# Kernel optimization log

Measured on AMD Instinct MI355X. Metric: run time of the kernel, lower is better.

The kernel has to match this reference:

```python
import jax, jax.numpy as jnp
import numpy as np

B, S, D, V, L = 8, 8192, 768, 64, 26  # batch, seq, hidden, symbol vocab, labels


def setup_inputs() -> dict:
    key = jax.random.key(0)
    k1, k2, k3 = jax.random.split(key, 3)
    hidden_states = jax.random.normal(k1, (B, S, D), dtype=jnp.float32)
    input_ids = jax.random.randint(k2, (B, S), 0, V, dtype=jnp.int32)
    W = jax.random.normal(k3, (L, D), dtype=jnp.float32) * 0.02
    b = jnp.zeros((L,), dtype=jnp.float32)
    return {"hidden_states": hidden_states, "W": W, "b": b, "input_ids": input_ids}


def reference(hidden_states, W, b, input_ids):
    # Per-batch, per-symbol mean pooling of hidden states, then linear classify.
    # Dense/padded equivalent of the torch per-symbol boolean-mask loop:
    # row (batch_b, symbol_v) = classifier(mean of hidden_states[b] where input_ids[b]==v),
    # masked to 0 for symbol 0 and for symbols absent in the sequence.
    Bv, Sv, Dv = hidden_states.shape
    seg = (input_ids + jnp.arange(Bv, dtype=input_ids.dtype)[:, None] * V).reshape(-1)
    flat_h = hidden_states.reshape(-1, Dv)
    sums = jax.ops.segment_sum(flat_h, seg, num_segments=Bv * V)            # [B*V, D]
    counts = jax.ops.segment_sum(
        jnp.ones((Bv * Sv,), dtype=hidden_states.dtype), seg, num_segments=Bv * V
    )                                                                        # [B*V]
    means = sums / jnp.maximum(counts, 1.0)[:, None]
    logits = means @ W.T + b                                                 # [B*V, L]
    present = (counts > 0) & ((jnp.arange(Bv * V) % V) > 0)                  # exclude symbol 0
    logits = jnp.where(present[:, None], logits, 0.0)
    return logits.reshape(Bv, V, -1)
```

## Files before the change

### kernel.cpp

```cpp
#include <hip/hip_runtime.h>

#define B_ 8
#define S_ 8192
#define D_ 768
#define V_ 64
#define L_ 26

typedef __attribute__((ext_vector_type(8))) short short8;
typedef __attribute__((ext_vector_type(4))) float floatx4;

#define TOKS 256
#define NSL  48

__global__ __launch_bounds__(256) void pool_mfma_kernel(
    const float* __restrict__ h, const int* __restrict__ ids,
    float* __restrict__ gsum)
{
    const int tid  = threadIdx.x;
    const int lane = tid & 63;
    const int wave = tid >> 6;
    const int nl   = lane & 15;
    const int quad = lane >> 4;

    const int b  = blockIdx.z;
    const int k0 = blockIdx.x * TOKS;
    const int n0 = blockIdx.y * (4 * NSL) + wave * NSL;

    const int*   idrow = ids + b * S_ + k0;
    const float* hrow  = h + ((size_t)b * S_ + k0) * D_ + n0;

    floatx4 acc[4][3];
    #pragma unroll
    for (int mt = 0; mt < 4; ++mt)
        #pragma unroll
        for (int nt = 0; nt < 3; ++nt) acc[mt][nt] = (floatx4)0.f;

    for (int ks = 0; ks < TOKS; ks += 32) {
        const int kb = ks + quad * 8;
        const int4* ip = (const int4*)(idrow + kb);
        const int4 i0 = ip[0], i1 = ip[1];
        const int idv[8] = {i0.x, i0.y, i0.z, i0.w, i1.x, i1.y, i1.z, i1.w};

        short8 afrag[4];
        #pragma unroll
        for (int mt = 0; mt < 4; ++mt) {
            const int m = mt * 16 + nl;
            #pragma unroll
            for (int j = 0; j < 8; ++j)
                afrag[mt][j] = (idv[j] == m) ? (short)0x3F80 : (short)0;
        }

        #pragma unroll
        for (int nt = 0; nt < 3; ++nt) {
            const float* bp = hrow + (size_t)kb * D_ + nt * 16 + nl;
            float f[8];
            #pragma unroll
            for (int j = 0; j < 8; ++j) f[j] = bp[(size_t)j * D_];
            short8 bhi, blo;
            #pragma unroll
            for (int j = 0; j < 8; ++j) {
                const unsigned u = __builtin_bit_cast(unsigned, f[j]);
                bhi[j] = (short)(u >> 16);
                const float hif = __builtin_bit_cast(float, u & 0xFFFF0000u);
                const float lof = f[j] - hif;
                blo[j] = (short)(__builtin_bit_cast(unsigned, lof) >> 16);
            }
            #pragma unroll
            for (int mt = 0; mt < 4; ++mt) {
                acc[mt][nt] = __builtin_amdgcn_mfma_f32_16x16x32_bf16(
                    afrag[mt], bhi, acc[mt][nt], 0, 0, 0);
                acc[mt][nt] = __builtin_amdgcn_mfma_f32_16x16x32_bf16(
                    afrag[mt], blo, acc[mt][nt], 0, 0, 0);
            }
        }
    }

    #pragma unroll
    for (int mt = 0; mt < 4; ++mt)
        #pragma unroll
        for (int nt = 0; nt < 3; ++nt)
            #pragma unroll
            for (int r = 0; r < 4; ++r) {
                const int v = mt * 16 + quad * 4 + r;
                const int d = n0 + nt * 16 + nl;
                unsafeAtomicAdd(&gsum[((size_t)b * V_ + v) * D_ + d],
                                acc[mt][nt][r]);
            }
}

__global__ __launch_bounds__(256) void hist_kernel(
    const int* __restrict__ ids, unsigned int* __restrict__ gcnt)
{
    __shared__ unsigned int cnt[V_];
    const int tid = threadIdx.x;
    const int b   = blockIdx.x >> 3;
    const int seg = blockIdx.x & 7;
    if (tid < V_) cnt[tid] = 0u;
    __syncthreads();
    const int per = S_ / 8;
    const int4* p = (const int4*)(ids + b * S_ + seg * per);
    for (int i = tid; i < per / 4; i += 256) {
        const int4 q = p[i];
        atomicAdd(&cnt[q.x], 1u); atomicAdd(&cnt[q.y], 1u);
        atomicAdd(&cnt[q.z], 1u); atomicAdd(&cnt[q.w], 1u);
    }
    __syncthreads();
    if (tid < V_ && cnt[tid]) atomicAdd(&gcnt[b * V_ + tid], cnt[tid]);
}

__global__ __launch_bounds__(256) void finalize_kernel(
    const float* __restrict__ gsum, const unsigned int* __restrict__ gcnt,
    const float* __restrict__ Wm, const float* __restrict__ bias,
    float* __restrict__ out)
{
    const int bv   = blockIdx.x;
    const int v    = bv & (V_ - 1);
    const int lane = threadIdx.x & 63;
    const int wave = threadIdx.x >> 6;

    const unsigned int c = gcnt[bv];
    const float inv = 1.f / (float)(c > 1u ? c : 1u);
    const bool present = (c > 0u) && (v > 0);

    float m[12];
    const float* srow = gsum + (size_t)bv * D_;
    #pragma unroll
    for (int j = 0; j < 12; ++j) m[j] = srow[lane + 64 * j] * inv;

    const int l0 = wave * 7;
    const int l1 = (l0 + 7 < L_) ? (l0 + 7) : L_;
    for (int l = l0; l < l1; ++l) {
        const float* wrow = Wm + l * D_;
        float p = 0.f;
        #pragma unroll
        for (int j = 0; j < 12; ++j) p += m[j] * wrow[lane + 64 * j];
        #pragma unroll
        for (int off = 32; off > 0; off >>= 1) p += __shfl_down(p, off);
        if (lane == 0) out[bv * L_ + l] = present ? (p + bias[l]) : 0.f;
    }
}

extern "C" void kernel_launch(void* const* d_in, const int* in_sizes, int n_in,
                              void* d_out, int out_size, void* d_ws, size_t ws_size,
                              hipStream_t stream) {
    const float* h    = (const float*)d_in[0];
    const float* Wm   = (const float*)d_in[1];
    const float* bias = (const float*)d_in[2];
    const int*   ids  = (const int*)d_in[3];
    float* out = (float*)d_out;

    float* gsum = (float*)d_ws;
    unsigned int* gcnt = (unsigned int*)(gsum + (size_t)B_ * V_ * D_);
    const size_t ws_needed = (size_t)B_ * V_ * D_ * sizeof(float)
                           + (size_t)B_ * V_ * sizeof(unsigned int);

    hipMemsetAsync(d_ws, 0, ws_needed, stream);

    hist_kernel<<<B_ * 8, 256, 0, stream>>>(ids, gcnt);

    dim3 grid1(S_ / TOKS, D_ / (4 * NSL), B_);
    pool_mfma_kernel<<<grid1, 256, 0, stream>>>(h, ids, gsum);

    finalize_kernel<<<B_ * V_, 256, 0, stream>>>(gsum, gcnt, Wm, bias, out);
}
```

Baseline: 313.5 us.

## Replace global atomics with per-slice partials and fuse histogram into pooling

The pooling kernel now writes per-slice partial sums into a workspace instead of doing global float atomics, which also removes the memset. It doubles tokens per block. The separate histogram kernel is folded into the pooling kernel, with per-slice counts written by the blockIdx.y==0 blocks. A new reduce-finalize kernel sums the 16 slices, computes means in shared memory and applies the classifier. The aim is to cut atomic contention and two launches, at the cost of extra partial-buffer traffic (16x B*V*D floats) and fewer blocks in the pooling grid.

```diff
diff --git a/kernel.cpp b/kernel.cpp
--- a/kernel.cpp
+++ b/kernel.cpp
@@ -9,25 +9,41 @@
 typedef __attribute__((ext_vector_type(8))) short short8;
 typedef __attribute__((ext_vector_type(4))) float floatx4;
 
-#define TOKS 256
+#define TOKS 512
+#define SLICES (S_ / TOKS)
 #define NSL  48
 
-__global__ __launch_bounds__(256) void pool_mfma_kernel(
+__global__ __launch_bounds__(256, 2) void pool_mfma_kernel(
     const float* __restrict__ h, const int* __restrict__ ids,
-    float* __restrict__ gsum)
+    float* __restrict__ part, unsigned int* __restrict__ cntpart)
 {
+    __shared__ unsigned int cnt[V_];
+
     const int tid  = threadIdx.x;
     const int lane = tid & 63;
     const int wave = tid >> 6;
     const int nl   = lane & 15;
     const int quad = lane >> 4;
 
-    const int b  = blockIdx.z;
-    const int k0 = blockIdx.x * TOKS;
-    const int n0 = blockIdx.y * (4 * NSL) + wave * NSL;
+    const int b     = blockIdx.z;
+    const int slice = blockIdx.x;
+    const int k0    = slice * TOKS;
+    const int n0    = blockIdx.y * (4 * NSL) + wave * NSL;
 
     const int*   idrow = ids + b * S_ + k0;
     const float* hrow  = h + ((size_t)b * S_ + k0) * D_ + n0;
+
+    if (blockIdx.y == 0) {
+        if (tid < V_) cnt[tid] = 0u;
+        __syncthreads();
+        if (tid < TOKS / 4) {
+            const int4 q = ((const int4*)idrow)[tid];
+            atomicAdd(&cnt[q.x], 1u); atomicAdd(&cnt[q.y], 1u);
+            atomicAdd(&cnt[q.z], 1u); atomicAdd(&cnt[q.w], 1u);
+        }
+        __syncthreads();
+        if (tid < V_) cntpart[(slice * B_ + b) * V_ + tid] = cnt[tid];
+    }
 
     floatx4 acc[4][3];
     #pragma unroll
@@ -75,6 +91,7 @@
         }
     }
 
+    float* pbase = part + ((size_t)(slice * B_ + b) * V_) * D_;
     #pragma unroll
     for (int mt = 0; mt < 4; ++mt)
         #pragma unroll
@@ -83,57 +100,56 @@
             for (int r = 0; r < 4; ++r) {
                 const int v = mt * 16 + quad * 4 + r;
                 const int d = n0 + nt * 16 + nl;
-                unsafeAtomicAdd(&gsum[((size_t)b * V_ + v) * D_ + d],
-                                acc[mt][nt][r]);
+                pbase[(size_t)v * D_ + d] = acc[mt][nt][r];
             }
 }
 
-__global__ __launch_bounds__(256) void hist_kernel(
-    const int* __restrict__ ids, unsigned int* __restrict__ gcnt)
-{
-    __shared__ unsigned int cnt[V_];
-    const int tid = threadIdx.x;
-    const int b   = blockIdx.x >> 3;
-    const int seg = blockIdx.x & 7;
-    if (tid < V_) cnt[tid] = 0u;
-    __syncthreads();
-    const int per = S_ / 8;
-    const int4* p = (const int4*)(ids + b * S_ + seg * per);
-    for (int i = tid; i < per / 4; i += 256) {
-        const int4 q = p[i];
-        atomicAdd(&cnt[q.x], 1u); atomicAdd(&cnt[q.y], 1u);
-        atomicAdd(&cnt[q.z], 1u); atomicAdd(&cnt[q.w], 1u);
-    }
-    __syncthreads();
-    if (tid < V_ && cnt[tid]) atomicAdd(&gcnt[b * V_ + tid], cnt[tid]);
-}
-
-__global__ __launch_bounds__(256) void finalize_kernel(
-    const float* __restrict__ gsum, const unsigned int* __restrict__ gcnt,
+__global__ __launch_bounds__(256) void reduce_finalize_kernel(
+    const float* __restrict__ part, const unsigned int* __restrict__ cntpart,
     const float* __restrict__ Wm, const float* __restrict__ bias,
     float* __restrict__ out)
 {
-    const int bv   = blockIdx.x;
-    const int v    = bv & (V_ - 1);
-    const int lane = threadIdx.x & 63;
-    const int wave = threadIdx.x >> 6;
+    __shared__ float mean[D_];
+    __shared__ unsigned int scnt;
 
-    const unsigned int c = gcnt[bv];
+    const int tid = threadIdx.x;
+    const int bv  = blockIdx.x;
+    const int b   = bv >> 6;
+    const int v   = bv & (V_ - 1);
+
+    if (tid == 0) scnt = 0u;
+    __syncthreads();
+    if (tid < SLICES)
+        atomicAdd(&scnt, cntpart[(tid * B_ + b) * V_ + v]);
+
+    float s[3];
+    #pragma unroll
+    for (int j = 0; j < 3; ++j) {
+        const int d = tid + j * 256;
+        float a = 0.f;
+        #pragma unroll
+        for (int sl = 0; sl < SLICES; ++sl)
+            a += part[((size_t)(sl * B_ + b) * V_ + v) * D_ + d];
+        s[j] = a;
+    }
+    __syncthreads();
+    const unsigned int c = scnt;
     const float inv = 1.f / (float)(c > 1u ? c : 1u);
+    #pragma unroll
+    for (int j = 0; j < 3; ++j) mean[tid + j * 256] = s[j] * inv;
+    __syncthreads();
+
     const bool present = (c > 0u) && (v > 0);
-
-    float m[12];
-    const float* srow = gsum + (size_t)bv * D_;
-    #pragma unroll
-    for (int j = 0; j < 12; ++j) m[j] = srow[lane + 64 * j] * inv;
-
-    const int l0 = wave * 7;
-    const int l1 = (l0 + 7 < L_) ? (l0 + 7) : L_;
-    for (int l = l0; l < l1; ++l) {
+    const int lane = tid & 63;
+    const int wave = tid >> 6;
+    for (int l = wave; l < L_; l += 4) {
         const float* wrow = Wm + l * D_;
         float p = 0.f;
         #pragma unroll
-        for (int j = 0; j < 12; ++j) p += m[j] * wrow[lane + 64 * j];
+        for (int j = 0; j < 12; ++j) {
+            const int d = lane + 64 * j;
+            p += mean[d] * wrow[d];
+        }
         #pragma unroll
         for (int off = 32; off > 0; off >>= 1) p += __shfl_down(p, off);
         if (lane == 0) out[bv * L_ + l] = present ? (p + bias[l]) : 0.f;
@@ -149,17 +165,13 @@
     const int*   ids  = (const int*)d_in[3];
     float* out = (float*)d_out;
 
-    float* gsum = (float*)d_ws;
-    unsigned int* gcnt = (unsigned int*)(gsum + (size_t)B_ * V_ * D_);
-    const size_t ws_needed = (size_t)B_ * V_ * D_ * sizeof(float)
-                           + (size_t)B_ * V_ * sizeof(unsigned int);
+    float* part = (float*)d_ws;
+    unsigned int* cntpart =
+        (unsigned int*)(part + (size_t)SLICES * B_ * V_ * D_);
 
-    hipMemsetAsync(d_ws, 0, ws_needed, stream);
+    dim3 grid1(SLICES, D_ / (4 * NSL), B_);
+    pool_mfma_kernel<<<grid1, 256, 0, stream>>>(h, ids, part, cntpart);
 
-    hist_kernel<<<B_ * 8, 256, 0, stream>>>(ids, gcnt);
-
-    dim3 grid1(S_ / TOKS, D_ / (4 * NSL), B_);
-    pool_mfma_kernel<<<grid1, 256, 0, stream>>>(h, ids, gsum);
-
-    finalize_kernel<<<B_ * V_, 256, 0, stream>>>(gsum, gcnt, Wm, bias, out);
+    reduce_finalize_kernel<<<B_ * V_, 256, 0, stream>>>(
+        part, cntpart, Wm, bias, out);
 }
```

Result: faster. 297.5 us (-5.1%).
